# Kernel optimization log

Hardware: AMD Instinct MI355X
Metric: run time of the kernel (lower is better)

The kernel has to match this reference:

```python
import jax, jax.numpy as jnp
import numpy as np

B, T, E, H = 4, 4096, 512, 64

def setup_inputs() -> dict:
    key = jax.random.key(0)
    k1, k2, k3, k4 = jax.random.split(key, 4)
    x = jax.random.normal(k1, (B, T, E), dtype=jnp.float32)
    # nn.Linear(E, H, bias=False) weight has shape [H, E]; y = x @ W.T
    Wq = jax.random.normal(k2, (H, E), dtype=jnp.float32) * (E ** -0.5)
    Wk = jax.random.normal(k3, (H, E), dtype=jnp.float32) * (E ** -0.5)
    Wv = jax.random.normal(k4, (H, E), dtype=jnp.float32) * (E ** -0.5)
    return {"x": x, "Wq": Wq, "Wk": Wk, "Wv": Wv}

def reference(x, Wq, Wk, Wv):
    # projections: [B, T, H]
    q = jnp.einsum('bte,he->bth', x, Wq)
    k = jnp.einsum('bte,he->bth', x, Wk)
    v = jnp.einsum('bte,he->bth', x, Wv)
    scale = 1.0 / jnp.sqrt(jnp.float32(q.shape[-1]))
    scores = jnp.einsum('bth,bsh->bts', q, k) * scale  # [B, T, T]
    t = scores.shape[-1]
    causal = jnp.tril(jnp.ones((t, t), dtype=bool))
    scores = jnp.where(causal, scores, -jnp.inf)
    probs = jax.nn.softmax(scores, axis=-1)
    # dropout p=0.0 (eval) -> identity
    return jnp.einsum('bts,bsh->bth', probs, v)
```

## Files before the change

### kernel.cpp

```cpp
#include <hip/hip_runtime.h>
#include <hip/hip_bf16.h>

#define Bn 4
#define Tn 4096
#define En 512
#define Hn 64
#define NEGINF -3e38f
#define QSCALE 0.1803368801f

typedef __attribute__((ext_vector_type(8))) __bf16 bf16x8;
typedef __attribute__((ext_vector_type(4))) __bf16 bf16x4;
typedef __attribute__((ext_vector_type(4))) float f32x4;

#define MFMA16(a, b, c) __builtin_amdgcn_mfma_f32_16x16x32_bf16(a, b, c, 0, 0, 0)

__device__ __forceinline__ float bf2f(unsigned short u) {
    union { unsigned u; float f; } v; v.u = ((unsigned)u) << 16;
    return v.f;
}
__device__ __forceinline__ unsigned cvtpk(float a, float b) {
    unsigned d;
    asm("v_cvt_pk_bf16_f32 %0, %1, %2" : "=v"(d) : "v"(a), "v"(b));
    return d;
}
__device__ __forceinline__ unsigned short f2bf(float f) {
    union { float f; unsigned u; } v; v.f = f;
    unsigned r = v.u + 0x7fffu + ((v.u >> 16) & 1u);
    return (unsigned short)(r >> 16);
}
__device__ __forceinline__ float exp2fast(float x) {
    float r;
    asm("v_exp_f32 %0, %1" : "=v"(r) : "v"(x));
    return r;
}
__device__ __forceinline__ void gl16(const void* g, void* l) {
    __builtin_amdgcn_global_load_lds(
        (const __attribute__((address_space(1))) unsigned int*)g,
        (__attribute__((address_space(3))) unsigned int*)l, 16, 0, 0);
}

__launch_bounds__(256, 2)
__global__ void proj(const float* __restrict__ x, const float* __restrict__ Wq,
                     const float* __restrict__ Wk, const float* __restrict__ Wv,
                     unsigned short* __restrict__ q16, unsigned short* __restrict__ k16,
                     unsigned short* __restrict__ vt16) {
    __shared__ __align__(16) unsigned char plds[2][28672];
    const int tid = threadIdx.x;
    const int w = tid >> 6, lane = tid & 63, r = lane & 15, g = lane >> 4;
    const int row0 = blockIdx.x * 32;
    const int rsel = (w & 1) * 16, csel = (w >> 1) * 96;

    const int srow = tid >> 3, skc = (tid & 7) * 8;
    const int sby = (tid & 7) * 16;

    f32x4 acc[6];
#pragma unroll
    for (int i = 0; i < 6; ++i) acc[i] = (f32x4){0.f, 0.f, 0.f, 0.f};

    {
        const float4* xp = (const float4*)&x[(row0 + srow) * En + skc];
        float4 f0 = xp[0], f1 = xp[1];
        union { bf16x8 v; unsigned u32[4]; } t;
        t.u32[0] = cvtpk(f0.x, f0.y); t.u32[1] = cvtpk(f0.z, f0.w);
        t.u32[2] = cvtpk(f1.x, f1.y); t.u32[3] = cvtpk(f1.z, f1.w);
        *(bf16x8*)&plds[0][srow * 128 + (sby ^ ((srow & 7) << 4))] = t.v;
#pragma unroll
        for (int c2 = 0; c2 < 6; ++c2) {
            const float* Ws = (c2 < 2) ? Wq : ((c2 < 4) ? Wk : Wv);
            int wr = (c2 & 1) * 32 + srow;
            const float4* wp = (const float4*)&Ws[wr * En + skc];
            float4 w0 = wp[0], w1 = wp[1];
            union { bf16x8 v; unsigned u32[4]; } tw;
            tw.u32[0] = cvtpk(w0.x, w0.y); tw.u32[1] = cvtpk(w0.z, w0.w);
            tw.u32[2] = cvtpk(w1.x, w1.y); tw.u32[3] = cvtpk(w1.z, w1.w);
            int wrow = c2 * 32 + srow;
            *(bf16x8*)&plds[0][4096 + wrow * 128 + (sby ^ ((wrow & 7) << 4))] = tw.v;
        }
    }
    __syncthreads();

    for (int s = 0; s < 8; ++s) {
        const int pp = s & 1;
        const bool more = (s < 7);
        float4 nf0, nf1;
        float4 nw0[6], nw1[6];
        if (more) {
            int k1 = (s + 1) * 64;
            const float4* xp = (const float4*)&x[(row0 + srow) * En + k1 + skc];
            nf0 = xp[0]; nf1 = xp[1];
#pragma unroll
            for (int c2 = 0; c2 < 6; ++c2) {
                const float* Ws = (c2 < 2) ? Wq : ((c2 < 4) ? Wk : Wv);
                int wr = (c2 & 1) * 32 + srow;
                const float4* wp = (const float4*)&Ws[wr * En + k1 + skc];
                nw0[c2] = wp[0]; nw1[c2] = wp[1];
            }
        }
        {
            const unsigned char* A = &plds[pp][0];
            const unsigned char* W = &plds[pp][4096];
            int arow = rsel + r, asw = (arow & 7) << 4;
            bf16x8 a0 = *(const bf16x8*)&A[arow * 128 + ((g * 16) ^ asw)];
            bf16x8 a1 = *(const bf16x8*)&A[arow * 128 + ((64 + g * 16) ^ asw)];
#pragma unroll
            for (int ct = 0; ct < 6; ++ct) {
                int wrow = csel + ct * 16 + r, wsw = (wrow & 7) << 4;
                bf16x8 b0 = *(const bf16x8*)&W[wrow * 128 + ((g * 16) ^ wsw)];
                bf16x8 b1 = *(const bf16x8*)&W[wrow * 128 + ((64 + g * 16) ^ wsw)];
                acc[ct] = MFMA16(a0, b0, acc[ct]);
                acc[ct] = MFMA16(a1, b1, acc[ct]);
            }
        }
        if (more) {
            unsigned char* D = &plds[pp ^ 1][0];
            union { bf16x8 v; unsigned u32[4]; } t;
            t.u32[0] = cvtpk(nf0.x, nf0.y); t.u32[1] = cvtpk(nf0.z, nf0.w);
            t.u32[2] = cvtpk(nf1.x, nf1.y); t.u32[3] = cvtpk(nf1.z, nf1.w);
            *(bf16x8*)&D[srow * 128 + (sby ^ ((srow & 7) << 4))] = t.v;
#pragma unroll
            for (int c2 = 0; c2 < 6; ++c2) {
                union { bf16x8 v; unsigned u32[4]; } tw;
                tw.u32[0] = cvtpk(nw0[c2].x, nw0[c2].y); tw.u32[1] = cvtpk(nw0[c2].z, nw0[c2].w);
                tw.u32[2] = cvtpk(nw1[c2].x, nw1[c2].y); tw.u32[3] = cvtpk(nw1[c2].z, nw1[c2].w);
                int wrow = c2 * 32 + srow;
                *(bf16x8*)&D[4096 + wrow * 128 + (sby ^ ((wrow & 7) << 4))] = tw.v;
            }
        }
        __syncthreads();
    }
#pragma unroll
    for (int ct = 0; ct < 6; ++ct) {
        int n = csel + ct * 16 + r;
#pragma unroll
        for (int reg = 0; reg < 4; ++reg) {
            int gr = row0 + rsel + g * 4 + reg;
            if (n < 64) {
                q16[gr * 64 + n] = f2bf(acc[ct][reg] * QSCALE);
            } else if (n < 128) {
                k16[gr * 64 + (n - 64)] = f2bf(acc[ct][reg]);
            } else {
                int h = n - 128; int bb = gr >> 12; int t = gr & 4095;
                vt16[((bb * 64 + h) << 12) + t] = f2bf(acc[ct][reg]);
            }
        }
    }
}

__launch_bounds__(256, 4)
__global__ void attnp(const unsigned short* __restrict__ q16, const unsigned short* __restrict__ k16,
                      const unsigned short* __restrict__ vt16,
                      unsigned short* __restrict__ po, float* __restrict__ lp) {
    __shared__ __align__(16) unsigned char lds[2][16384];

    const int tid = threadIdx.x;
    const int w = tid >> 6, lane = tid & 63, r = lane & 15, g = lane >> 4;
    const int bid = blockIdx.x;
    const int page = bid >> 8, idx = bid & 255;
    const int s5 = idx >> 3, b = (idx >> 1) & 3, q1 = idx & 1;
    const int jt = (page & 1) ? s5 : 31 - s5;
    const int piece = ((page & 1) << 2) | ((page >> 1) << 1) | q1;
    const size_t kbase = (size_t)b * Tn;
    const int q0 = jt * 128;
    const int nt = 2 * (jt + 1);
    const int t0 = (piece * nt) >> 3;
    const int tEnd = ((piece + 1) * nt) >> 3;
    const int wq0 = q0 + w * 32;

    const unsigned short* Kb = k16 + kbase * 64;
    const unsigned short* Vb = vt16 + ((size_t)(b * 64) << 12);

    const int srl = lane >> 3, scb = (lane & 7) * 16;

    bf16x8 bq[2][2];
#pragma unroll
    for (int qf = 0; qf < 2; ++qf) {
        const unsigned short* qp = &q16[(kbase + wq0 + qf * 16 + r) * 64 + g * 8];
        bq[qf][0] = *(const bf16x8*)qp;
        bq[qf][1] = *(const bf16x8*)(qp + 32);
    }

    f32x4 o[2][4];
#pragma unroll
    for (int qf = 0; qf < 2; ++qf)
#pragma unroll
        for (int i = 0; i < 4; ++i) o[qf][i] = (f32x4){0.f, 0.f, 0.f, 0.f};
    float l_[2] = {0.f, 0.f};

    if (tEnd > t0) {
        int kv0 = t0 * 64;
        unsigned char* D = &lds[t0 & 1][0];
#pragma unroll
        for (int i = 0; i < 4; ++i) {
            int cc = w * 4 + i;
            if (cc < 8) {
                int row = cc * 8 + srl, sw = (row & 7) << 4;
                gl16((const char*)Kb + (size_t)(kv0 + row) * 128 + (scb ^ sw), D + cc * 1024);
            } else {
                int h = (cc - 8) * 8 + srl, sw = (h & 7) << 4;
                gl16((const char*)Vb + (size_t)h * 8192 + (size_t)kv0 * 2 + (scb ^ sw), D + cc * 1024);
            }
        }
    }

    for (int it = t0; it < tEnd; ++it) {
        const int pp = it & 1;
        asm volatile("s_waitcnt vmcnt(0)" ::: "memory");
        __builtin_amdgcn_s_barrier();
        __builtin_amdgcn_sched_barrier(0);
        if (it + 1 < tEnd) {
            int nkv = (it + 1) * 64;
            unsigned char* D = &lds[pp ^ 1][0];
#pragma unroll
            for (int i = 0; i < 4; ++i) {
                int cc = w * 4 + i;
                if (cc < 8) {
                    int row = cc * 8 + srl, sw = (row & 7) << 4;
                    gl16((const char*)Kb + (size_t)(nkv + row) * 128 + (scb ^ sw), D + cc * 1024);
                } else {
                    int h = (cc - 8) * 8 + srl, sw = (h & 7) << 4;
                    gl16((const char*)Vb + (size_t)h * 8192 + (size_t)nkv * 2 + (scb ^ sw), D + cc * 1024);
                }
            }
        }
        const int kv0 = it * 64;
        if (kv0 <= wq0 + 31) {
            const unsigned char* K = &lds[pp][0];
            const unsigned char* V = &lds[pp][8192];
            f32x4 s4[2][4];
            __builtin_amdgcn_s_setprio(1);
#pragma unroll
            for (int ct = 0; ct < 4; ++ct) {
                int row = ct * 16 + r;
                int base = row * 128, sw = (row & 7) << 4;
                bf16x8 ak0 = *(const bf16x8*)&K[base + ((g * 16) ^ sw)];
                bf16x8 ak1 = *(const bf16x8*)&K[base + ((64 + g * 16) ^ sw)];
#pragma unroll
                for (int qf = 0; qf < 2; ++qf) {
                    f32x4 t = (f32x4){0.f, 0.f, 0.f, 0.f};
                    t = MFMA16(ak0, bq[qf][0], t);
                    t = MFMA16(ak1, bq[qf][1], t);
                    s4[qf][ct] = t;
                }
            }
            __builtin_amdgcn_s_setprio(0);
            if (kv0 + 63 > wq0) {
#pragma unroll
                for (int qf = 0; qf < 2; ++qf) {
                    int qq = wq0 + qf * 16 + r;
#pragma unroll
                    for (int ct = 0; ct < 4; ++ct)
#pragma unroll
                        for (int reg = 0; reg < 4; ++reg) {
                            int kv = kv0 + ct * 16 + g * 4 + reg;
                            if (kv > qq) s4[qf][ct][reg] = NEGINF;
                        }
                }
            }
            union { bf16x8 v; unsigned u32[4]; } pk[2][2];
#pragma unroll
            for (int qf = 0; qf < 2; ++qf) {
#pragma unroll
                for (int ct = 0; ct < 4; ++ct)
#pragma unroll
                    for (int reg = 0; reg < 4; ++reg)
                        s4[qf][ct][reg] = exp2fast(s4[qf][ct][reg]);
                l_[qf] += ((s4[qf][0][0] + s4[qf][0][1]) + (s4[qf][0][2] + s4[qf][0][3])) +
                          ((s4[qf][1][0] + s4[qf][1][1]) + (s4[qf][1][2] + s4[qf][1][3])) +
                          ((s4[qf][2][0] + s4[qf][2][1]) + (s4[qf][2][2] + s4[qf][2][3])) +
                          ((s4[qf][3][0] + s4[qf][3][1]) + (s4[qf][3][2] + s4[qf][3][3]));
#pragma unroll
                for (int kf = 0; kf < 2; ++kf) {
                    pk[qf][kf].u32[0] = cvtpk(s4[qf][kf * 2][0], s4[qf][kf * 2][1]);
                    pk[qf][kf].u32[1] = cvtpk(s4[qf][kf * 2][2], s4[qf][kf * 2][3]);
                    pk[qf][kf].u32[2] = cvtpk(s4[qf][kf * 2 + 1][0], s4[qf][kf * 2 + 1][1]);
                    pk[qf][kf].u32[3] = cvtpk(s4[qf][kf * 2 + 1][2], s4[qf][kf * 2 + 1][3]);
                }
            }
            __builtin_amdgcn_s_setprio(1);
#pragma unroll
            for (int cth = 0; cth < 4; ++cth) {
                int h = cth * 16 + r;
                int vb = h * 128, sw2 = (h & 7) << 4;
#pragma unroll
                for (int kf = 0; kf < 2; ++kf) {
                    int off = kf * 64 + g * 8;
                    union { bf16x8 v; bf16x4 h4[2]; } vv;
                    vv.h4[0] = *(const bf16x4*)&V[vb + (off ^ sw2)];
                    vv.h4[1] = *(const bf16x4*)&V[vb + ((off + 32) ^ sw2)];
                    o[0][cth] = MFMA16(pk[0][kf].v, vv.v, o[0][cth]);
                    o[1][cth] = MFMA16(pk[1][kf].v, vv.v, o[1][cth]);
                }
            }
            __builtin_amdgcn_s_setprio(0);
        }
    }

    const size_t qb = (size_t)piece * 16384 + b * 4096;
#pragma unroll
    for (int qf = 0; qf < 2; ++qf) {
#pragma unroll
        for (int cth = 0; cth < 4; ++cth)
#pragma unroll
            for (int reg = 0; reg < 4; ++reg)
                po[(qb + wq0 + qf * 16 + g * 4 + reg) * 64 + cth * 16 + r] = f2bf(o[qf][cth][reg]);
        lp[(qb + wq0 + qf * 16 + r) * 4 + g] = l_[qf];
    }
}

__global__ void merge(const unsigned short* __restrict__ po, const float* __restrict__ lp,
                      float* __restrict__ out) {
    int t = blockIdx.x * 256 + threadIdx.x;
    int q = t >> 3, c8 = (t & 7) * 8;
    float L = 0.f;
#pragma unroll
    for (int c = 0; c < 8; ++c)
#pragma unroll
        for (int gg = 0; gg < 4; ++gg)
            L += lp[((size_t)c * 16384 + q) * 4 + gg];
    float inv = 1.0f / L;
    float acc[8] = {0.f, 0.f, 0.f, 0.f, 0.f, 0.f, 0.f, 0.f};
#pragma unroll
    for (int c = 0; c < 8; ++c) {
        union { uint4 v; unsigned short u[8]; } ld;
        ld.v = *(const uint4*)&po[((size_t)c * 16384 + q) * 64 + c8];
#pragma unroll
        for (int j = 0; j < 8; ++j) acc[j] += bf2f(ld.u[j]);
    }
    float4* op = (float4*)&out[(size_t)q * 64 + c8];
    op[0] = (float4){acc[0] * inv, acc[1] * inv, acc[2] * inv, acc[3] * inv};
    op[1] = (float4){acc[4] * inv, acc[5] * inv, acc[6] * inv, acc[7] * inv};
}

extern "C" void kernel_launch(void* const* d_in, const int* in_sizes, int n_in,
                              void* d_out, int out_size, void* d_ws, size_t ws_size,
                              hipStream_t stream) {
    const float* x  = (const float*)d_in[0];
    const float* Wq = (const float*)d_in[1];
    const float* Wk = (const float*)d_in[2];
    const float* Wv = (const float*)d_in[3];
    float* out = (float*)d_out;
    char* ws = (char*)d_ws;

    unsigned short* q16 = (unsigned short*)ws;
    unsigned short* k16 = (unsigned short*)(ws + 2097152);
    unsigned short* v16 = (unsigned short*)(ws + 4194304);
    unsigned short* po  = (unsigned short*)(ws + 6291456);
    float*          lp  = (float*)(ws + 23068672);

    hipLaunchKernelGGL(proj, dim3(512), dim3(256), 0, stream, x, Wq, Wk, Wv, q16, k16, v16);
    hipLaunchKernelGGL(attnp, dim3(1024), dim3(256), 0, stream, q16, k16, v16, po, lp);
    hipLaunchKernelGGL(merge, dim3(512), dim3(256), 0, stream, po, lp, out);
}
```

Measured before the change: 42.42 us.

## Pre-convert weights to bf16 and stream them into LDS with direct global loads

Adds a small kernel that converts Wq/Wk/Wv to one packed bf16 buffer before the projection. The projection kernel then fetches weight tiles with global_load_lds, writing straight into swizzled LDS. This drops the per-block fp32 weight loads, register staging and conversions that every one of the 512 blocks repeated. The loop barrier becomes an explicit waitcnt plus s_barrier at the top of each step. The cost is an extra kernel launch and a workspace reshuffle.

```diff
diff --git a/kernel.cpp b/kernel.cpp
--- a/kernel.cpp
+++ b/kernel.cpp
@@ -39,9 +39,17 @@
         (__attribute__((address_space(3))) unsigned int*)l, 16, 0, 0);
 }
 
+__global__ void wcvt(const float* __restrict__ Wq, const float* __restrict__ Wk,
+                     const float* __restrict__ Wv, unsigned short* __restrict__ Wo) {
+    int i = blockIdx.x * 256 + threadIdx.x;
+    int mat = i >> 15;
+    int off = i & 32767;
+    const float* s = (mat == 0) ? Wq : ((mat == 1) ? Wk : Wv);
+    Wo[i] = f2bf(s[off]);
+}
+
 __launch_bounds__(256, 2)
-__global__ void proj(const float* __restrict__ x, const float* __restrict__ Wq,
-                     const float* __restrict__ Wk, const float* __restrict__ Wv,
+__global__ void proj(const float* __restrict__ x, const unsigned short* __restrict__ Wo,
                      unsigned short* __restrict__ q16, unsigned short* __restrict__ k16,
                      unsigned short* __restrict__ vt16) {
     __shared__ __align__(16) unsigned char plds[2][28672];
@@ -52,49 +60,46 @@
 
     const int srow = tid >> 3, skc = (tid & 7) * 8;
     const int sby = (tid & 7) * 16;
+    const int srl = lane >> 3, scb = (lane & 7) * 16;
 
     f32x4 acc[6];
 #pragma unroll
     for (int i = 0; i < 6; ++i) acc[i] = (f32x4){0.f, 0.f, 0.f, 0.f};
 
     {
+#pragma unroll
+        for (int i = 0; i < 6; ++i) {
+            int cc = w * 6 + i;
+            int wrow = cc * 8 + srl;
+            gl16((const char*)Wo + (size_t)wrow * 1024 + (scb ^ ((wrow & 7) << 4)),
+                 &plds[0][4096 + cc * 1024]);
+        }
         const float4* xp = (const float4*)&x[(row0 + srow) * En + skc];
         float4 f0 = xp[0], f1 = xp[1];
         union { bf16x8 v; unsigned u32[4]; } t;
         t.u32[0] = cvtpk(f0.x, f0.y); t.u32[1] = cvtpk(f0.z, f0.w);
         t.u32[2] = cvtpk(f1.x, f1.y); t.u32[3] = cvtpk(f1.z, f1.w);
         *(bf16x8*)&plds[0][srow * 128 + (sby ^ ((srow & 7) << 4))] = t.v;
-#pragma unroll
-        for (int c2 = 0; c2 < 6; ++c2) {
-            const float* Ws = (c2 < 2) ? Wq : ((c2 < 4) ? Wk : Wv);
-            int wr = (c2 & 1) * 32 + srow;
-            const float4* wp = (const float4*)&Ws[wr * En + skc];
-            float4 w0 = wp[0], w1 = wp[1];
-            union { bf16x8 v; unsigned u32[4]; } tw;
-            tw.u32[0] = cvtpk(w0.x, w0.y); tw.u32[1] = cvtpk(w0.z, w0.w);
-            tw.u32[2] = cvtpk(w1.x, w1.y); tw.u32[3] = cvtpk(w1.z, w1.w);
-            int wrow = c2 * 32 + srow;
-            *(bf16x8*)&plds[0][4096 + wrow * 128 + (sby ^ ((wrow & 7) << 4))] = tw.v;
-        }
-    }
-    __syncthreads();
+    }
 
     for (int s = 0; s < 8; ++s) {
         const int pp = s & 1;
         const bool more = (s < 7);
+        asm volatile("s_waitcnt vmcnt(0) lgkmcnt(0)" ::: "memory");
+        __builtin_amdgcn_s_barrier();
+        __builtin_amdgcn_sched_barrier(0);
         float4 nf0, nf1;
-        float4 nw0[6], nw1[6];
         if (more) {
             int k1 = (s + 1) * 64;
+#pragma unroll
+            for (int i = 0; i < 6; ++i) {
+                int cc = w * 6 + i;
+                int wrow = cc * 8 + srl;
+                gl16((const char*)Wo + (size_t)wrow * 1024 + k1 * 2 + (scb ^ ((wrow & 7) << 4)),
+                     &plds[pp ^ 1][4096 + cc * 1024]);
+            }
             const float4* xp = (const float4*)&x[(row0 + srow) * En + k1 + skc];
             nf0 = xp[0]; nf1 = xp[1];
-#pragma unroll
-            for (int c2 = 0; c2 < 6; ++c2) {
-                const float* Ws = (c2 < 2) ? Wq : ((c2 < 4) ? Wk : Wv);
-                int wr = (c2 & 1) * 32 + srow;
-                const float4* wp = (const float4*)&Ws[wr * En + k1 + skc];
-                nw0[c2] = wp[0]; nw1[c2] = wp[1];
-            }
         }
         {
             const unsigned char* A = &plds[pp][0];
@@ -112,21 +117,11 @@
             }
         }
         if (more) {
-            unsigned char* D = &plds[pp ^ 1][0];
             union { bf16x8 v; unsigned u32[4]; } t;
             t.u32[0] = cvtpk(nf0.x, nf0.y); t.u32[1] = cvtpk(nf0.z, nf0.w);
             t.u32[2] = cvtpk(nf1.x, nf1.y); t.u32[3] = cvtpk(nf1.z, nf1.w);
-            *(bf16x8*)&D[srow * 128 + (sby ^ ((srow & 7) << 4))] = t.v;
-#pragma unroll
-            for (int c2 = 0; c2 < 6; ++c2) {
-                union { bf16x8 v; unsigned u32[4]; } tw;
-                tw.u32[0] = cvtpk(nw0[c2].x, nw0[c2].y); tw.u32[1] = cvtpk(nw0[c2].z, nw0[c2].w);
-                tw.u32[2] = cvtpk(nw1[c2].x, nw1[c2].y); tw.u32[3] = cvtpk(nw1[c2].z, nw1[c2].w);
-                int wrow = c2 * 32 + srow;
-                *(bf16x8*)&D[4096 + wrow * 128 + (sby ^ ((wrow & 7) << 4))] = tw.v;
-            }
-        }
-        __syncthreads();
+            *(bf16x8*)&plds[pp ^ 1][srow * 128 + (sby ^ ((srow & 7) << 4))] = t.v;
+        }
     }
 #pragma unroll
     for (int ct = 0; ct < 6; ++ct) {
@@ -341,13 +336,15 @@
     float* out = (float*)d_out;
     char* ws = (char*)d_ws;
 
-    unsigned short* q16 = (unsigned short*)ws;
-    unsigned short* k16 = (unsigned short*)(ws + 2097152);
-    unsigned short* v16 = (unsigned short*)(ws + 4194304);
-    unsigned short* po  = (unsigned short*)(ws + 6291456);
-    float*          lp  = (float*)(ws + 23068672);
-
-    hipLaunchKernelGGL(proj, dim3(512), dim3(256), 0, stream, x, Wq, Wk, Wv, q16, k16, v16);
+    unsigned short* Wo  = (unsigned short*)ws;
+    unsigned short* q16 = (unsigned short*)(ws + 196608);
+    unsigned short* k16 = (unsigned short*)(ws + 2293760);
+    unsigned short* v16 = (unsigned short*)(ws + 4390912);
+    unsigned short* po  = (unsigned short*)(ws + 6488064);
+    float*          lp  = (float*)(ws + 23265280);
+
+    hipLaunchKernelGGL(wcvt, dim3(384), dim3(256), 0, stream, Wq, Wk, Wv, Wo);
+    hipLaunchKernelGGL(proj, dim3(512), dim3(256), 0, stream, x, Wo, q16, k16, v16);
     hipLaunchKernelGGL(attnp, dim3(1024), dim3(256), 0, stream, q16, k16, v16, po, lp);
     hipLaunchKernelGGL(merge, dim3(512), dim3(256), 0, stream, po, lp, out);
 }
```

After: 42.86 us. No clear change (+1.0%).
